# Kernel optimization log

Measured on AMD Instinct MI355X. Metric: run time of the kernel, lower is better.

The kernel has to match this reference:

```python
import jax, jax.numpy as jnp
import numpy as np

B, S, D_MODEL, H, DK, DV, DOUT = 8, 2048, 1024, 1, 512, 512, 1024
EPS = 1e-6
TEMP = DK ** 0.5


def _ln(x, g, b):
    # LayerNorm over last dim, eps=1e-6, affine
    m = jnp.mean(x, axis=-1, keepdims=True)
    v = jnp.mean((x - m) ** 2, axis=-1, keepdims=True)
    return (x - m) * jax.lax.rsqrt(v + EPS) * g + b


def setup_inputs() -> dict:
    key = jax.random.key(0)
    ks = jax.random.split(key, 16)
    s = 0.02
    return {
        "q": jax.random.normal(ks[0], (B, S, D_MODEL), jnp.float32),
        "k": jax.random.normal(ks[1], (B, S, D_MODEL), jnp.float32),
        "v": jax.random.normal(ks[2], (B, S, D_MODEL), jnp.float32),
        "mask": jnp.ones((B, S, S), jnp.int32),
        "Wq": jax.random.normal(ks[3], (D_MODEL, H * DK), jnp.float32) * s,
        "bq": jnp.zeros((H * DK,), jnp.float32),
        "Wk": jax.random.normal(ks[4], (D_MODEL, H * DK), jnp.float32) * s,
        "bk": jnp.zeros((H * DK,), jnp.float32),
        "Wv": jax.random.normal(ks[5], (D_MODEL, H * DV), jnp.float32) * s,
        "bv": jnp.zeros((H * DV,), jnp.float32),
        "g_q": jnp.ones((H * DK,), jnp.float32),
        "be_q": jnp.zeros((H * DK,), jnp.float32),
        "g_k": jnp.ones((H * DK,), jnp.float32),
        "be_k": jnp.zeros((H * DK,), jnp.float32),
        "g_v": jnp.ones((H * DV,), jnp.float32),
        "be_v": jnp.zeros((H * DV,), jnp.float32),
        "W1": jax.random.normal(ks[6], (H * DV, H * DV), jnp.float32) * s,
        "b1": jnp.zeros((H * DV,), jnp.float32),
        "W2": jax.random.normal(ks[7], (H * DV, DOUT), jnp.float32) * s,
        "b2": jnp.zeros((DOUT,), jnp.float32),
    }


def reference(q, k, v, mask, Wq, bq, Wk, bk, Wv, bv, g_q, be_q, g_k, be_k, g_v, be_v, W1, b1, W2, b2):
    # QKV projections, viewed as (B, S, H, d)
    qp = (q @ Wq + bq).reshape(B, S, H, DK)
    kp = (k @ Wk + bk).reshape(B, S, H, DK)
    vp = (v @ Wv + bv).reshape(B, S, H, DV)
    residual = qp
    # per-(token,head) LayerNorm over last dim (valid only because H == 1 in source)
    qn = jnp.swapaxes(_ln(qp, g_q, be_q), 1, 2)  # (B, H, S, DK)
    kn = jnp.swapaxes(_ln(kp, g_k, be_k), 1, 2)
    vn = jnp.swapaxes(_ln(vp, g_v, be_v), 1, 2)
    # scaled dot-product attention with mask
    scores = jnp.einsum('bhqd,bhkd->bhqk', qn / TEMP, kn)
    scores = jnp.where(mask[:, None, :, :] == 0, -1e9, scores)
    attn = jax.nn.softmax(scores, axis=-1)
    out = jnp.einsum('bhqk,bhkd->bhqd', attn, vn)
    out = jnp.swapaxes(out, 1, 2).reshape(B, S, H * DV)
    # trailing 2-layer MLP
    out = jax.nn.relu(out @ W1 + b1) @ W2 + b2
    return (out, residual, jnp.squeeze(attn))
```

## Files before the change

### kernel.cpp

```cpp
#include <hip/hip_runtime.h>
#include <hip/hip_bf16.h>

typedef __attribute__((ext_vector_type(8))) short short8;
typedef __attribute__((ext_vector_type(4))) short short4v;
typedef __attribute__((ext_vector_type(4))) float f32x4;

#define INV_TEMP 0.044194173824159216f

__device__ __forceinline__ ushort f2bf(float f) {
  unsigned u = __float_as_uint(f);
  unsigned r = (u + 0x7FFFu + ((u >> 16) & 1u)) >> 16;
  return (ushort)r;
}
__device__ __forceinline__ float bf2f(ushort u) {
  union { unsigned i; float f; } x; x.i = ((unsigned)u) << 16; return x.f;
}

__device__ __forceinline__ void gload_lds16(const void* g, void* l) {
  __builtin_amdgcn_global_load_lds(
      (const __attribute__((address_space(1))) unsigned int*)(unsigned long long)(uintptr_t)g,
      (__attribute__((address_space(3))) unsigned int*)(unsigned)(uintptr_t)l,
      16, 0, 0);
}

__global__ __launch_bounds__(256)
void transpose_cvt_all(const float* __restrict__ Wq, const float* __restrict__ Wk,
                       const float* __restrict__ Wv, const float* __restrict__ W1,
                       const float* __restrict__ W2,
                       ushort* __restrict__ Tq, ushort* __restrict__ Tk,
                       ushort* __restrict__ Tv, ushort* __restrict__ T1,
                       ushort* __restrict__ T2) {
  const int z = blockIdx.z;
  const int K = (z < 3) ? 1024 : 512;
  const int N = (z == 4) ? 1024 : 512;
  if (blockIdx.x * 32 >= N || blockIdx.y * 32 >= K) return;
  const float* W = z == 0 ? Wq : (z == 1 ? Wk : (z == 2 ? Wv : (z == 3 ? W1 : W2)));
  ushort* WT = z == 0 ? Tq : (z == 1 ? Tk : (z == 2 ? Tv : (z == 3 ? T1 : T2)));
  __shared__ float tile[32][33];
  const int n0 = blockIdx.x * 32, k0 = blockIdx.y * 32;
  const int tx = threadIdx.x & 31, ty = threadIdx.x >> 5;
  #pragma unroll
  for (int i = ty; i < 32; i += 8)
    tile[i][tx] = W[(long)(k0 + i) * N + n0 + tx];
  __syncthreads();
  #pragma unroll
  for (int i = ty; i < 32; i += 8)
    WT[(long)(n0 + i) * K + k0 + tx] = f2bf(tile[tx][i]);
}

__global__ __launch_bounds__(256)
void transpose_bf16(const ushort* __restrict__ in, ushort* __restrict__ out, int S, int D) {
  __shared__ ushort tile[32][33];
  const ushort* inb = in + (long)blockIdx.z * S * D;
  ushort* outb = out + (long)blockIdx.z * S * D;
  const int d0 = blockIdx.x * 32, s0 = blockIdx.y * 32;
  const int tx = threadIdx.x & 31, ty = threadIdx.x >> 5;
  #pragma unroll
  for (int i = ty; i < 32; i += 8)
    tile[i][tx] = inb[(long)(s0 + i) * D + d0 + tx];
  __syncthreads();
  #pragma unroll
  for (int i = ty; i < 32; i += 8)
    outb[(long)(d0 + i) * S + s0 + tx] = tile[tx][i];
}

__global__ __launch_bounds__(256)
void ln3_kernel(const float* __restrict__ Xq, const ushort* __restrict__ Xk,
                const ushort* __restrict__ Xv,
                const float* __restrict__ gq, const float* __restrict__ beq,
                const float* __restrict__ gk, const float* __restrict__ bek,
                const float* __restrict__ gv, const float* __restrict__ bev,
                ushort* __restrict__ Oq, ushort* __restrict__ Ok, ushort* __restrict__ Ov) {
  const int which = blockIdx.y;
  const float* g = which == 0 ? gq : (which == 1 ? gk : gv);
  const float* be = which == 0 ? beq : (which == 1 ? bek : bev);
  ushort* out = which == 0 ? Oq : (which == 1 ? Ok : Ov);
  const float scale = which == 0 ? INV_TEMP : 1.0f;

  const int row = blockIdx.x * 4 + (threadIdx.x >> 6);
  const int lane = threadIdx.x & 63;
  f32x4 v0, v1;
  if (which == 0) {
    const float* x = Xq + (long)row * 512 + lane * 8;
    v0 = *(const f32x4*)x;
    v1 = *(const f32x4*)(x + 4);
  } else {
    const ushort* x = (which == 1 ? Xk : Xv) + (long)row * 512 + lane * 8;
    short8 vv = *(const short8*)x;
    #pragma unroll
    for (int j = 0; j < 4; j++) { v0[j] = bf2f((ushort)vv[j]); v1[j] = bf2f((ushort)vv[4 + j]); }
  }
  float s = v0[0]+v0[1]+v0[2]+v0[3]+v1[0]+v1[1]+v1[2]+v1[3];
  float ss = v0[0]*v0[0]+v0[1]*v0[1]+v0[2]*v0[2]+v0[3]*v0[3]
           + v1[0]*v1[0]+v1[1]*v1[1]+v1[2]*v1[2]+v1[3]*v1[3];
  #pragma unroll
  for (int off = 32; off; off >>= 1) { s += __shfl_xor(s, off); ss += __shfl_xor(ss, off); }
  const float mean = s * (1.0f/512.0f);
  const float var  = ss * (1.0f/512.0f) - mean*mean;
  const float rs = rsqrtf(var + 1e-6f);
  f32x4 g0 = *(const f32x4*)(g + lane*8);
  f32x4 g1 = *(const f32x4*)(g + lane*8 + 4);
  f32x4 b0 = *(const f32x4*)(be + lane*8);
  f32x4 b1 = *(const f32x4*)(be + lane*8 + 4);
  union { short8 v; ushort u[8]; } o;
  #pragma unroll
  for (int j = 0; j < 4; j++) o.u[j]     = f2bf(((v0[j]-mean)*rs*g0[j] + b0[j]) * scale);
  #pragma unroll
  for (int j = 0; j < 4; j++) o.u[4 + j] = f2bf(((v1[j]-mean)*rs*g1[j] + b1[j]) * scale);
  *(short8*)(out + (long)row * 512 + lane * 8) = o.v;
}

__global__ __launch_bounds__(256)
void invz_reduce(const float* __restrict__ partial, float* __restrict__ invZ) {
  const int r = blockIdx.x * 256 + threadIdx.x;
  const int zb = r >> 11, s = r & 2047;
  float z = 0.f;
  #pragma unroll
  for (int j = 0; j < 16; j++) z += partial[((zb * 16 + j) << 11) + s];
  invZ[r] = 1.0f / z;
}

template<int EPI, bool HAS_BIAS, bool OUT_BF16, bool A_F32>
__global__ __launch_bounds__(512)
void gemm_tn_pipe(const void* __restrict__ Av, const ushort* __restrict__ Bt,
                  const float* __restrict__ bias, const int* __restrict__ mask,
                  float* __restrict__ Cf, ushort* __restrict__ Cb,
                  float* __restrict__ partial, const float* __restrict__ invZ,
                  int M, int N, int K,
                  long sA, long sB, long sC, long sMask) {
  __shared__ ushort As[2][128 * 64];
  __shared__ ushort Bs[2][128 * 64];
  __shared__ float zloc[128];
  const int tid = threadIdx.x;
  const int lane = tid & 63;
  const int wave = tid >> 6;
  const int wr = wave >> 2;
  const int wc = wave & 3;

  const int gx = gridDim.x, gy = gridDim.y;
  int lin = blockIdx.x + gx * (blockIdx.y + gy * blockIdx.z);
  const int nwg = gx * gy * (int)gridDim.z;
  int swz = lin;
  if ((nwg & 7) == 0) {
    const int q8 = nwg >> 3;
    swz = (lin & 7) * q8 + (lin >> 3);
  }
  const int bx = swz % gx;
  const int tmp = swz / gx;
  const int by = tmp % gy;
  const int bz = tmp / gy;

  const long zb = bz;
  const ushort* Ab = (const ushort*)Av + zb * sA + (long)by * 128 * K;
  const float*  Af = (const float*)Av + zb * sA + (long)by * 128 * K;
  const ushort* Bb = Bt + zb * sB + (long)bx * 128 * K;
  const int rowbase0 = by * 128;
  const int nt = K >> 6;

  if constexpr (EPI == 3) {
    if (tid < 128) zloc[tid] = invZ[zb * 2048 + rowbase0 + tid];
  }

  auto stage = [&](int buf, int t) {
    const long kt = (long)t << 6;
    if constexpr (A_F32) {
      const int c0 = tid, c1 = 512 + tid;
      const float* p0 = Af + (long)(c0 >> 3) * K + kt + (c0 & 7) * 8;
      const float* p1 = Af + (long)(c1 >> 3) * K + kt + (c1 & 7) * 8;
      f32x4 a00 = *(const f32x4*)p0;
      f32x4 a01 = *(const f32x4*)(p0 + 4);
      f32x4 a10 = *(const f32x4*)p1;
      f32x4 a11 = *(const f32x4*)(p1 + 4);
      #pragma unroll
      for (int e = 0; e < 2; e++) {
        const int c = e * 512 + tid;
        const int row = c >> 3, g = c & 7, gsrc = g ^ (row & 7);
        gload_lds16(Bb + (long)row * K + kt + gsrc * 8, (char*)Bs[buf] + c * 16);
      }
      union { short8 s; ushort u[8]; } o0, o1;
      #pragma unroll
      for (int j = 0; j < 4; j++) {
        o0.u[j] = f2bf(a00[j]); o0.u[4 + j] = f2bf(a01[j]);
        o1.u[j] = f2bf(a10[j]); o1.u[4 + j] = f2bf(a11[j]);
      }
      const int r0 = c0 >> 3, g0 = c0 & 7, r1 = c1 >> 3, g1 = c1 & 7;
      *(short8*)((char*)As[buf] + ((r0 << 7) | ((g0 << 4) ^ ((r0 & 7) << 4)))) = o0.s;
      *(short8*)((char*)As[buf] + ((r1 << 7) | ((g1 << 4) ^ ((r1 & 7) << 4)))) = o1.s;
    } else {
      #pragma unroll
      for (int e = 0; e < 2; e++) {
        const int c = e * 512 + tid;
        const int row = c >> 3, g = c & 7, gsrc = g ^ (row & 7);
        gload_lds16(Ab + (long)row * K + kt + gsrc * 8, (char*)As[buf] + c * 16);
        gload_lds16(Bb + (long)row * K + kt + gsrc * 8, (char*)Bs[buf] + c * 16);
      }
    }
  };

  f32x4 acc[4][2];
  #pragma unroll
  for (int m = 0; m < 4; m++)
    #pragma unroll
    for (int n = 0; n < 2; n++)
      acc[m][n] = f32x4{0.f, 0.f, 0.f, 0.f};

  stage(0, 0);
  stage(1, 1);

  for (int t = 0; t < nt; ++t) {
    const int buf = t & 1;
    if (t == nt - 1) {
      asm volatile("s_waitcnt vmcnt(0)" ::: "memory");
    } else if constexpr (A_F32) {
      asm volatile("s_waitcnt vmcnt(2)" ::: "memory");
    } else {
      asm volatile("s_waitcnt vmcnt(4)" ::: "memory");
    }
    __builtin_amdgcn_s_barrier();
    __builtin_amdgcn_sched_barrier(0);

    if constexpr (EPI == 3) {
      if ((t >> 3) == bx) {
        #pragma unroll
        for (int e = 0; e < 2; e++) {
          const int c = e * 512 + tid;
          const int row = c >> 3, g = c & 7;
          short8 p8 = *(const short8*)((const char*)As[buf] +
                       ((row << 7) | ((g ^ (row & 7)) << 4)));
          const float iz = zloc[row];
          f32x4 o0, o1;
          #pragma unroll
          for (int jj = 0; jj < 4; jj++) {
            o0[jj] = bf2f((ushort)p8[jj]) * iz;
            o1[jj] = bf2f((ushort)p8[4 + jj]) * iz;
          }
          float* dst = Cf + zb * 4194304L + (long)(rowbase0 + row) * 2048 + (t << 6) + g * 8;
          *(f32x4*)dst = o0;
          *(f32x4*)(dst + 4) = o1;
        }
      }
    }

    #pragma unroll
    for (int ks = 0; ks < 2; ks++) {
      short8 af[4], bfr[2];
      const int kb = ks * 64 + ((lane >> 4) << 4);
      #pragma unroll
      for (int m = 0; m < 4; m++) {
        const int row = wr * 64 + m * 16 + (lane & 15);
        af[m] = *(const short8*)((const char*)As[buf] +
                 ((row << 7) | (kb ^ ((row & 7) << 4))));
      }
      #pragma unroll
      for (int n = 0; n < 2; n++) {
        const int col = wc * 32 + n * 16 + (lane & 15);
        bfr[n] = *(const short8*)((const char*)Bs[buf] +
                  ((col << 7) | (kb ^ ((col & 7) << 4))));
      }
      #pragma unroll
      for (int m = 0; m < 4; m++)
        #pragma unroll
        for (int n = 0; n < 2; n++)
          acc[m][n] = __builtin_amdgcn_mfma_f32_16x16x32_bf16(af[m], bfr[n], acc[m][n], 0, 0, 0);
    }
    __builtin_amdgcn_sched_barrier(0);
    __builtin_amdgcn_s_barrier();
    __builtin_amdgcn_sched_barrier(0);
    if (t + 2 < nt) stage(buf, t + 2);
  }

  const int colbase = bx * 128 + wc * 32;
  const int rowbase = by * 128 + wr * 64;
  const int c_lane = lane & 15;
  const int r_lane = (lane >> 4) << 2;

  float rs_acc[4][4];
  if constexpr (EPI == 2) {
    #pragma unroll
    for (int m = 0; m < 4; m++)
      #pragma unroll
      for (int r4 = 0; r4 < 4; r4++) rs_acc[m][r4] = 0.f;
  }

  #pragma unroll
  for (int n = 0; n < 2; n++) {
    const int col = colbase + n * 16 + c_lane;
    const float bv = HAS_BIAS ? bias[col] : 0.0f;
    #pragma unroll
    for (int m = 0; m < 4; m++) {
      const int rbase = rowbase + m * 16 + r_lane;
      #pragma unroll
      for (int r4 = 0; r4 < 4; r4++) {
        const int row = rbase + r4;
        float vv = acc[m][n][r4] + bv;
        if constexpr (EPI == 1) vv = fmaxf(vv, 0.0f);
        if constexpr (EPI == 2) {
          const int mk = mask[zb * sMask + (long)row * N + col];
          vv = mk ? __expf(vv) : 0.0f;
          rs_acc[m][r4] += vv;
        }
        if constexpr (EPI == 3) vv *= zloc[wr * 64 + m * 16 + r_lane + r4];
        const long off = zb * sC + (long)row * N + col;
        if constexpr (OUT_BF16) Cb[off] = f2bf(vv);
        else                    Cf[off] = vv;
      }
    }
  }

  if constexpr (EPI == 2) {
    __syncthreads();
    float (*red)[128] = (float(*)[128])As;
    #pragma unroll
    for (int m = 0; m < 4; m++)
      #pragma unroll
      for (int r4 = 0; r4 < 4; r4++) {
        float vsum = rs_acc[m][r4];
        vsum += __shfl_xor(vsum, 1);
        vsum += __shfl_xor(vsum, 2);
        vsum += __shfl_xor(vsum, 4);
        vsum += __shfl_xor(vsum, 8);
        if (c_lane == 0) red[wc][wr * 64 + m * 16 + r_lane + r4] = vsum;
      }
    __syncthreads();
    if (tid < 128)
      partial[((long)zb * 16 + bx) * 2048 + by * 128 + tid] =
          red[0][tid] + red[1][tid] + red[2][tid] + red[3][tid];
  }
}

extern "C" void kernel_launch(void* const* d_in, const int* in_sizes, int n_in,
                              void* d_out, int out_size, void* d_ws, size_t ws_size,
                              hipStream_t stream) {
  const float* q    = (const float*)d_in[0];
  const float* k    = (const float*)d_in[1];
  const float* v    = (const float*)d_in[2];
  const int*   mask = (const int*)d_in[3];
  const float* Wq   = (const float*)d_in[4];
  const float* bq   = (const float*)d_in[5];
  const float* Wk   = (const float*)d_in[6];
  const float* bk   = (const float*)d_in[7];
  const float* Wv   = (const float*)d_in[8];
  const float* bv   = (const float*)d_in[9];
  const float* g_q  = (const float*)d_in[10];
  const float* be_q = (const float*)d_in[11];
  const float* g_k  = (const float*)d_in[12];
  const float* be_k = (const float*)d_in[13];
  const float* g_v  = (const float*)d_in[14];
  const float* be_v = (const float*)d_in[15];
  const float* W1   = (const float*)d_in[16];
  const float* b1   = (const float*)d_in[17];
  const float* W2   = (const float*)d_in[18];
  const float* b2   = (const float*)d_in[19];

  float* out_mlp  = (float*)d_out;
  float* out_res  = out_mlp + 16777216L;
  float* out_attn = out_res + 8388608L;

  char* w = (char*)d_ws;
  ushort* qn      = (ushort*)(w);
  ushort* kn      = (ushort*)(w + 16777216UL);
  ushort* kp_bf   = (ushort*)(w + 33554432UL);
  ushort* vp_bf   = (ushort*)(w + 50331648UL);
  ushort* attn_bf = (ushort*)(w + 33554432UL);
  ushort* vn      = (ushort*)(w + 100663296UL);
  ushort* vnT     = (ushort*)(w + 117440512UL);
  ushort* pv      = (ushort*)(w + 134217728UL);
  ushort* h       = (ushort*)(w + 150994944UL);
  ushort* wqT     = (ushort*)(w + 167772160UL);
  ushort* wkT     = (ushort*)(w + 168820736UL);
  ushort* wvT     = (ushort*)(w + 169869312UL);
  ushort* w1T     = (ushort*)(w + 170917888UL);
  ushort* w2T     = (ushort*)(w + 171442176UL);
  float*  partial = (float*)(w + 172490752UL);
  float*  invZ    = (float*)(w + 173539328UL);

  dim3 blk(256);
  dim3 blk512(512);

  transpose_cvt_all<<<dim3(32, 32, 5), blk, 0, stream>>>(
      Wq, Wk, Wv, W1, W2, wqT, wkT, wvT, w1T, w2T);

  gemm_tn_pipe<0, true, false, true><<<dim3(4, 128, 1), blk512, 0, stream>>>(
      q, wqT, bq, nullptr, out_res, nullptr, nullptr, nullptr,
      16384, 512, 1024, 0, 0, 0, 0);
  gemm_tn_pipe<0, true, true, true><<<dim3(4, 128, 1), blk512, 0, stream>>>(
      k, wkT, bk, nullptr, nullptr, kp_bf, nullptr, nullptr,
      16384, 512, 1024, 0, 0, 0, 0);
  gemm_tn_pipe<0, true, true, true><<<dim3(4, 128, 1), blk512, 0, stream>>>(
      v, wvT, bv, nullptr, nullptr, vp_bf, nullptr, nullptr,
      16384, 512, 1024, 0, 0, 0, 0);

  ln3_kernel<<<dim3(4096, 3), blk, 0, stream>>>(
      out_res, kp_bf, vp_bf, g_q, be_q, g_k, be_k, g_v, be_v, qn, kn, vn);

  transpose_bf16<<<dim3(16, 64, 8), blk, 0, stream>>>(vn, vnT, 2048, 512);

  gemm_tn_pipe<2, false, true, false><<<dim3(16, 16, 8), blk512, 0, stream>>>(
      qn, kn, nullptr, mask, nullptr, attn_bf, partial, nullptr,
      2048, 2048, 512,
      (long)2048 * 512, (long)2048 * 512, (long)2048 * 2048, (long)2048 * 2048);

  invz_reduce<<<64, blk, 0, stream>>>(partial, invZ);

  gemm_tn_pipe<3, false, true, false><<<dim3(4, 16, 8), blk512, 0, stream>>>(
      attn_bf, vnT, nullptr, nullptr, out_attn, pv, nullptr, invZ,
      2048, 512, 2048,
      (long)2048 * 2048, (long)512 * 2048, (long)2048 * 512, 0);

  gemm_tn_pipe<1, true, true, false><<<dim3(4, 128, 1), blk512, 0, stream>>>(
      pv, w1T, b1, nullptr, nullptr, h, nullptr, nullptr,
      16384, 512, 512, 0, 0, 0, 0);
  gemm_tn_pipe<0, true, false, false><<<dim3(8, 128, 1), blk512, 0, stream>>>(
      h, w2T, b2, nullptr, out_mlp, nullptr, nullptr, nullptr,
      16384, 1024, 512, 0, 0, 0, 0);
}
```

Baseline: 376.5 us.

## Use 4-wave GEMM blocks, batch QKV projections, fold invZ reduce into PV GEMM

Result: no change. 370.0 us (-1.7%).

```diff
diff --git a/kernel.cpp b/kernel.cpp
--- a/kernel.cpp
+++ b/kernel.cpp
@@ -110,22 +110,16 @@
   *(short8*)(out + (long)row * 512 + lane * 8) = o.v;
 }
 
+template<int EPI, bool HAS_BIAS, bool OUT_BF16, bool A_F32>
 __global__ __launch_bounds__(256)
-void invz_reduce(const float* __restrict__ partial, float* __restrict__ invZ) {
-  const int r = blockIdx.x * 256 + threadIdx.x;
-  const int zb = r >> 11, s = r & 2047;
-  float z = 0.f;
-  #pragma unroll
-  for (int j = 0; j < 16; j++) z += partial[((zb * 16 + j) << 11) + s];
-  invZ[r] = 1.0f / z;
-}
-
-template<int EPI, bool HAS_BIAS, bool OUT_BF16, bool A_F32>
-__global__ __launch_bounds__(512)
 void gemm_tn_pipe(const void* __restrict__ Av, const ushort* __restrict__ Bt,
                   const float* __restrict__ bias, const int* __restrict__ mask,
                   float* __restrict__ Cf, ushort* __restrict__ Cb,
-                  float* __restrict__ partial, const float* __restrict__ invZ,
+                  float* __restrict__ partial,
+                  const float* __restrict__ A2, const float* __restrict__ A3,
+                  const ushort* __restrict__ Bt2, const ushort* __restrict__ Bt3,
+                  const float* __restrict__ bias2, const float* __restrict__ bias3,
+                  ushort* __restrict__ Cb2,
                   int M, int N, int K,
                   long sA, long sB, long sC, long sMask) {
   __shared__ ushort As[2][128 * 64];
@@ -134,8 +128,8 @@
   const int tid = threadIdx.x;
   const int lane = tid & 63;
   const int wave = tid >> 6;
-  const int wr = wave >> 2;
-  const int wc = wave & 3;
+  const int wr = wave >> 1;
+  const int wc = wave & 1;
 
   const int gx = gridDim.x, gy = gridDim.y;
   int lin = blockIdx.x + gx * (blockIdx.y + gy * blockIdx.z);
@@ -151,45 +145,63 @@
   const int bz = tmp / gy;
 
   const long zb = bz;
+  const float* Afp;
+  const ushort* Bb;
+  const float* bias_p = bias;
+  if constexpr (EPI == 4) {
+    Afp = (bz == 0 ? (const float*)Av : (bz == 1 ? A2 : A3)) + (long)by * 128 * K;
+    Bb = (bz == 0 ? Bt : (bz == 1 ? Bt2 : Bt3)) + (long)bx * 128 * K;
+    bias_p = bz == 0 ? bias : (bz == 1 ? bias2 : bias3);
+  } else {
+    Afp = (const float*)Av + zb * sA + (long)by * 128 * K;
+    Bb = Bt + zb * sB + (long)bx * 128 * K;
+  }
   const ushort* Ab = (const ushort*)Av + zb * sA + (long)by * 128 * K;
-  const float*  Af = (const float*)Av + zb * sA + (long)by * 128 * K;
-  const ushort* Bb = Bt + zb * sB + (long)bx * 128 * K;
   const int rowbase0 = by * 128;
   const int nt = K >> 6;
 
   if constexpr (EPI == 3) {
-    if (tid < 128) zloc[tid] = invZ[zb * 2048 + rowbase0 + tid];
+    if (tid < 128) {
+      float z = 0.f;
+      #pragma unroll
+      for (int j = 0; j < 16; j++)
+        z += partial[((long)(zb * 16 + j)) * 2048 + rowbase0 + tid];
+      zloc[tid] = 1.0f / z;
+    }
   }
 
   auto stage = [&](int buf, int t) {
     const long kt = (long)t << 6;
     if constexpr (A_F32) {
-      const int c0 = tid, c1 = 512 + tid;
-      const float* p0 = Af + (long)(c0 >> 3) * K + kt + (c0 & 7) * 8;
-      const float* p1 = Af + (long)(c1 >> 3) * K + kt + (c1 & 7) * 8;
-      f32x4 a00 = *(const f32x4*)p0;
-      f32x4 a01 = *(const f32x4*)(p0 + 4);
-      f32x4 a10 = *(const f32x4*)p1;
-      f32x4 a11 = *(const f32x4*)(p1 + 4);
-      #pragma unroll
-      for (int e = 0; e < 2; e++) {
-        const int c = e * 512 + tid;
+      f32x4 a[4][2];
+      #pragma unroll
+      for (int i = 0; i < 4; i++) {
+        const int c = i * 256 + tid;
+        const int row = c >> 3, g = c & 7;
+        const float* p = Afp + (long)row * K + kt + g * 8;
+        a[i][0] = *(const f32x4*)p;
+        a[i][1] = *(const f32x4*)(p + 4);
+      }
+      #pragma unroll
+      for (int i = 0; i < 4; i++) {
+        const int c = i * 256 + tid;
         const int row = c >> 3, g = c & 7, gsrc = g ^ (row & 7);
         gload_lds16(Bb + (long)row * K + kt + gsrc * 8, (char*)Bs[buf] + c * 16);
       }
-      union { short8 s; ushort u[8]; } o0, o1;
-      #pragma unroll
-      for (int j = 0; j < 4; j++) {
-        o0.u[j] = f2bf(a00[j]); o0.u[4 + j] = f2bf(a01[j]);
-        o1.u[j] = f2bf(a10[j]); o1.u[4 + j] = f2bf(a11[j]);
-      }
-      const int r0 = c0 >> 3, g0 = c0 & 7, r1 = c1 >> 3, g1 = c1 & 7;
-      *(short8*)((char*)As[buf] + ((r0 << 7) | ((g0 << 4) ^ ((r0 & 7) << 4)))) = o0.s;
-      *(short8*)((char*)As[buf] + ((r1 << 7) | ((g1 << 4) ^ ((r1 & 7) << 4)))) = o1.s;
+      #pragma unroll
+      for (int i = 0; i < 4; i++) {
+        const int c = i * 256 + tid;
+        const int row = c >> 3, g = c & 7;
+        union { short8 s; ushort u[8]; } o;
+        #pragma unroll
+        for (int j = 0; j < 4; j++) { o.u[j] = f2bf(a[i][0][j]); o.u[4 + j] = f2bf(a[i][1][j]); }
+        *(short8*)((char*)As[buf] + ((row << 7) | ((g << 4) ^ ((row & 7) << 4)))) = o.s;
+      }
+      asm volatile("s_waitcnt lgkmcnt(0)" ::: "memory");
     } else {
       #pragma unroll
-      for (int e = 0; e < 2; e++) {
-        const int c = e * 512 + tid;
+      for (int i = 0; i < 4; i++) {
+        const int c = i * 256 + tid;
         const int row = c >> 3, g = c & 7, gsrc = g ^ (row & 7);
         gload_lds16(Ab + (long)row * K + kt + gsrc * 8, (char*)As[buf] + c * 16);
         gload_lds16(Bb + (long)row * K + kt + gsrc * 8, (char*)Bs[buf] + c * 16);
@@ -197,11 +209,11 @@
     }
   };
 
-  f32x4 acc[4][2];
+  f32x4 acc[4][4];
   #pragma unroll
   for (int m = 0; m < 4; m++)
     #pragma unroll
-    for (int n = 0; n < 2; n++)
+    for (int n = 0; n < 4; n++)
       acc[m][n] = f32x4{0.f, 0.f, 0.f, 0.f};
 
   stage(0, 0);
@@ -212,9 +224,9 @@
     if (t == nt - 1) {
       asm volatile("s_waitcnt vmcnt(0)" ::: "memory");
     } else if constexpr (A_F32) {
-      asm volatile("s_waitcnt vmcnt(2)" ::: "memory");
+      asm volatile("s_waitcnt vmcnt(4)" ::: "memory");
     } else {
-      asm volatile("s_waitcnt vmcnt(4)" ::: "memory");
+      asm volatile("s_waitcnt vmcnt(8)" ::: "memory");
     }
     __builtin_amdgcn_s_barrier();
     __builtin_amdgcn_sched_barrier(0);
@@ -222,8 +234,8 @@
     if constexpr (EPI == 3) {
       if ((t >> 3) == bx) {
         #pragma unroll
-        for (int e = 0; e < 2; e++) {
-          const int c = e * 512 + tid;
+        for (int e = 0; e < 4; e++) {
+          const int c = e * 256 + tid;
           const int row = c >> 3, g = c & 7;
           short8 p8 = *(const short8*)((const char*)As[buf] +
                        ((row << 7) | ((g ^ (row & 7)) << 4)));
@@ -243,7 +255,7 @@
 
     #pragma unroll
     for (int ks = 0; ks < 2; ks++) {
-      short8 af[4], bfr[2];
+      short8 af[4], bfr[4];
       const int kb = ks * 64 + ((lane >> 4) << 4);
       #pragma unroll
       for (int m = 0; m < 4; m++) {
@@ -252,15 +264,15 @@
                  ((row << 7) | (kb ^ ((row & 7) << 4))));
       }
       #pragma unroll
-      for (int n = 0; n < 2; n++) {
-        const int col = wc * 32 + n * 16 + (lane & 15);
+      for (int n = 0; n < 4; n++) {
+        const int col = wc * 64 + n * 16 + (lane & 15);
         bfr[n] = *(const short8*)((const char*)Bs[buf] +
                   ((col << 7) | (kb ^ ((col & 7) << 4))));
       }
       #pragma unroll
       for (int m = 0; m < 4; m++)
         #pragma unroll
-        for (int n = 0; n < 2; n++)
+        for (int n = 0; n < 4; n++)
           acc[m][n] = __builtin_amdgcn_mfma_f32_16x16x32_bf16(af[m], bfr[n], acc[m][n], 0, 0, 0);
     }
     __builtin_amdgcn_sched_barrier(0);
@@ -269,7 +281,7 @@
     if (t + 2 < nt) stage(buf, t + 2);
   }
 
-  const int colbase = bx * 128 + wc * 32;
+  const int colbase = bx * 128 + wc * 64;
   const int rowbase = by * 128 + wr * 64;
   const int c_lane = lane & 15;
   const int r_lane = (lane >> 4) << 2;
@@ -283,9 +295,9 @@
   }
 
   #pragma unroll
-  for (int n = 0; n < 2; n++) {
+  for (int n = 0; n < 4; n++) {
     const int col = colbase + n * 16 + c_lane;
-    const float bv = HAS_BIAS ? bias[col] : 0.0f;
+    const float bv = HAS_BIAS ? bias_p[col] : 0.0f;
     #pragma unroll
     for (int m = 0; m < 4; m++) {
       const int rbase = rowbase + m * 16 + r_lane;
@@ -301,8 +313,15 @@
         }
         if constexpr (EPI == 3) vv *= zloc[wr * 64 + m * 16 + r_lane + r4];
         const long off = zb * sC + (long)row * N + col;
-        if constexpr (OUT_BF16) Cb[off] = f2bf(vv);
-        else                    Cf[off] = vv;
+        if constexpr (EPI == 4) {
+          if (bz == 0) Cf[off] = vv;
+          else if (bz == 1) Cb[off] = f2bf(vv);
+          else Cb2[off] = f2bf(vv);
+        } else if constexpr (OUT_BF16) {
+          Cb[off] = f2bf(vv);
+        } else {
+          Cf[off] = vv;
+        }
       }
     }
   }
@@ -323,8 +342,7 @@
       }
     __syncthreads();
     if (tid < 128)
-      partial[((long)zb * 16 + bx) * 2048 + by * 128 + tid] =
-          red[0][tid] + red[1][tid] + red[2][tid] + red[3][tid];
+      partial[((long)zb * 16 + bx) * 2048 + by * 128 + tid] = red[0][tid] + red[1][tid];
   }
 }
 
@@ -372,22 +390,15 @@
   ushort* w1T     = (ushort*)(w + 170917888UL);
   ushort* w2T     = (ushort*)(w + 171442176UL);
   float*  partial = (float*)(w + 172490752UL);
-  float*  invZ    = (float*)(w + 173539328UL);
 
   dim3 blk(256);
-  dim3 blk512(512);
 
   transpose_cvt_all<<<dim3(32, 32, 5), blk, 0, stream>>>(
       Wq, Wk, Wv, W1, W2, wqT, wkT, wvT, w1T, w2T);
 
-  gemm_tn_pipe<0, true, false, true><<<dim3(4, 128, 1), blk512, 0, stream>>>(
-      q, wqT, bq, nullptr, out_res, nullptr, nullptr, nullptr,
-      16384, 512, 1024, 0, 0, 0, 0);
-  gemm_tn_pipe<0, true, true, true><<<dim3(4, 128, 1), blk512, 0, stream>>>(
-      k, wkT, bk, nullptr, nullptr, kp_bf, nullptr, nullptr,
-      16384, 512, 1024, 0, 0, 0, 0);
-  gemm_tn_pipe<0, true, true, true><<<dim3(4, 128, 1), blk512, 0, stream>>>(
-      v, wvT, bv, nullptr, nullptr, vp_bf, nullptr, nullptr,
+  gemm_tn_pipe<4, true, false, true><<<dim3(4, 128, 3), blk, 0, stream>>>(
+      q, wqT, bq, nullptr, out_res, kp_bf, nullptr,
+      k, v, wkT, wvT, bk, bv, vp_bf,
       16384, 512, 1024, 0, 0, 0, 0);
 
   ln3_kernel<<<dim3(4096, 3), blk, 0, stream>>>(
@@ -395,22 +406,24 @@
 
   transpose_bf16<<<dim3(16, 64, 8), blk, 0, stream>>>(vn, vnT, 2048, 512);
 
-  gemm_tn_pipe<2, false, true, false><<<dim3(16, 16, 8), blk512, 0, stream>>>(
-      qn, kn, nullptr, mask, nullptr, attn_bf, partial, nullptr,
+  gemm_tn_pipe<2, false, true, false><<<dim3(16, 16, 8), blk, 0, stream>>>(
+      qn, kn, nullptr, mask, nullptr, attn_bf, partial,
+      nullptr, nullptr, nullptr, nullptr, nullptr, nullptr, nullptr,
       2048, 2048, 512,
       (long)2048 * 512, (long)2048 * 512, (long)2048 * 2048, (long)2048 * 2048);
 
-  invz_reduce<<<64, blk, 0, stream>>>(partial, invZ);
-
-  gemm_tn_pipe<3, false, true, false><<<dim3(4, 16, 8), blk512, 0, stream>>>(
-      attn_bf, vnT, nullptr, nullptr, out_attn, pv, nullptr, invZ,
+  gemm_tn_pipe<3, false, true, false><<<dim3(4, 16, 8), blk, 0, stream>>>(
+      attn_bf, vnT, nullptr, nullptr, out_attn, pv, partial,
+      nullptr, nullptr, nullptr, nullptr, nullptr, nullptr, nullptr,
       2048, 512, 2048,
       (long)2048 * 2048, (long)512 * 2048, (long)2048 * 512, 0);
 
-  gemm_tn_pipe<1, true, true, false><<<dim3(4, 128, 1), blk512, 0, stream>>>(
-      pv, w1T, b1, nullptr, nullptr, h, nullptr, nullptr,
+  gemm_tn_pipe<1, true, true, false><<<dim3(4, 128, 1), blk, 0, stream>>>(
+      pv, w1T, b1, nullptr, nullptr, h, nullptr,
+      nullptr, nullptr, nullptr, nullptr, nullptr, nullptr, nullptr,
       16384, 512, 512, 0, 0, 0, 0);
-  gemm_tn_pipe<0, true, false, false><<<dim3(8, 128, 1), blk512, 0, stream>>>(
-      h, w2T, b2, nullptr, out_mlp, nullptr, nullptr, nullptr,
+  gemm_tn_pipe<0, true, false, false><<<dim3(8, 128, 1), blk, 0, stream>>>(
+      h, w2T, b2, nullptr, out_mlp, nullptr, nullptr,
+      nullptr, nullptr, nullptr, nullptr, nullptr, nullptr, nullptr,
       16384, 1024, 512, 0, 0, 0, 0);
 }
```
